# Optimization experiments

Measured on AMD Instinct MI355X. Metric: run time of the kernel, lower is better.

The kernel has to match this reference:

```python
import jax, jax.numpy as jnp
import numpy as np

CHEB_K = 3
EMBED_DIM = 16
N_NODES = 2048
DIM = 64


def setup_inputs() -> dict:
    key = jax.random.key(0)
    k1, k2, k3, k4 = jax.random.split(key, 4)
    B, N, T, D = 16, N_NODES, 12, DIM
    x = jax.random.normal(k1, (B, N, T, D), dtype=jnp.float32)
    node_embeddings = jax.random.normal(k2, (N, EMBED_DIM), dtype=jnp.float32)
    # xavier-uniform-ish init for pools
    wp_bound = float(np.sqrt(6.0 / (EMBED_DIM * CHEB_K * D + D)))
    weights_pool = jax.random.uniform(k3, (EMBED_DIM, CHEB_K, D, D), dtype=jnp.float32,
                                      minval=-wp_bound, maxval=wp_bound)
    bias_pool = jax.random.uniform(k4, (EMBED_DIM, D), dtype=jnp.float32)
    return {"x": x, "node_embeddings": node_embeddings,
            "weights_pool": weights_pool, "bias_pool": bias_pool}


def reference(x, node_embeddings, weights_pool, bias_pool):
    B, N, T, D = x.shape
    cheb_k = weights_pool.shape[1]
    # [B,N,T,D] -> [B*T, N, D]
    xr = jnp.transpose(x, (0, 2, 1, 3)).reshape(B * T, N, D)
    # adaptive adjacency: row-softmax of relu gram matrix  [N,N]
    supports = jax.nn.softmax(jax.nn.relu(node_embeddings @ node_embeddings.T), axis=1)
    # Chebyshev polynomial basis of the adaptive support
    support_set = [jnp.eye(N, dtype=supports.dtype), supports]
    for _ in range(2, cheb_k):
        support_set.append(2.0 * supports @ support_set[-1] - support_set[-2])
    supports_k = jnp.stack(support_set, axis=0)  # [K,N,N]
    # hypernetwork: per-node weights/bias from embeddings
    weights = jnp.einsum('nd,dkio->nkio', node_embeddings, weights_pool)  # [N,K,D,D]
    bias = node_embeddings @ bias_pool  # [N,D]
    # graph conv: gather K-hop aggregates, then per-node grouped GEMM
    x_g = jnp.einsum('knm,bmc->bnkc', supports_k, xr)  # [B*T,N,K,D]
    x_gconv = jnp.einsum('bnki,nkio->bno', x_g, weights) + bias  # [B*T,N,D]
    return jnp.transpose(x_gconv.reshape(B, T, N, D), (0, 2, 1, 3))
```

## Files before the change

### kernel.cpp

```cpp
#include <hip/hip_runtime.h>
#include <hip/hip_bf16.h>

#define N_NODES 2048
#define EMB 16
#define NT 12
#define BT 192
#define C_COLS 12288
#define TD 768
#define BSTRIDE (N_NODES * TD)
#define KDIM 2048

typedef unsigned short u16;
typedef unsigned int u32;
typedef __attribute__((ext_vector_type(8))) __bf16 bf16x8;
typedef __attribute__((ext_vector_type(8))) u16 u16x8;
typedef __attribute__((ext_vector_type(4))) float f32x4;

__device__ __forceinline__ u16 f2bfu(float f) {
    u32 u = __float_as_uint(f);
    return (u16)((u + 0x7FFFu + ((u >> 16) & 1u)) >> 16);
}
__device__ __forceinline__ float bfu2f(u16 h) {
    return __uint_as_float(((u32)h) << 16);
}

__device__ __forceinline__ void gl2lds16(const void* g, void* l) {
    __builtin_amdgcn_global_load_lds(
        (const __attribute__((address_space(1))) u32*)g,
        (__attribute__((address_space(3))) u32*)l, 16, 0, 0);
}

__device__ __forceinline__ int cswz(int col, int row) {
    return (col & ~63) | ((((col >> 3) ^ row) & 7) << 3) | (col & 7);
}

__global__ void supports_kernel(const float* __restrict__ E, u16* __restrict__ Sb)
{
    __shared__ float en[EMB];
    __shared__ float red[256];
    const int n = blockIdx.x;
    const int tid = threadIdx.x;
    if (tid < EMB) en[tid] = E[n * EMB + tid];
    __syncthreads();

    float v[8];
    float mx = 0.0f;
    #pragma unroll
    for (int j = 0; j < 8; ++j) {
        const int m = tid + j * 256;
        const float* em = E + m * EMB;
        float acc = 0.f;
        #pragma unroll
        for (int d = 0; d < EMB; ++d) acc += en[d] * em[d];
        acc = fmaxf(acc, 0.f);
        v[j] = acc;
        mx = fmaxf(mx, acc);
    }
    red[tid] = mx;
    __syncthreads();
    for (int s = 128; s > 0; s >>= 1) {
        if (tid < s) red[tid] = fmaxf(red[tid], red[tid + s]);
        __syncthreads();
    }
    mx = red[0];
    __syncthreads();

    float sum = 0.f;
    #pragma unroll
    for (int j = 0; j < 8; ++j) { v[j] = __expf(v[j] - mx); sum += v[j]; }
    red[tid] = sum;
    __syncthreads();
    for (int s = 128; s > 0; s >>= 1) {
        if (tid < s) red[tid] += red[tid + s];
        __syncthreads();
    }
    const float inv = 1.f / red[0];
    #pragma unroll
    for (int j = 0; j < 8; ++j)
        Sb[(size_t)n * KDIM + tid + j * 256] = f2bfu(v[j] * inv);
}

__global__ void supports2_kernel(const float* __restrict__ E, u16* __restrict__ Sb)
{
    __shared__ float en[EMB];
    __shared__ float red[256];
    const int n = blockIdx.x;
    const int tid = threadIdx.x;
    if (tid < EMB) en[tid] = E[n * EMB + tid];
    __syncthreads();

    float v[8];
    float mx = 0.0f;
    #pragma unroll
    for (int j = 0; j < 8; ++j) {
        const int m = tid + j * 256;
        const float* em = E + m * EMB;
        float acc = 0.f;
        #pragma unroll
        for (int d = 0; d < EMB; ++d) acc += en[d] * em[d];
        acc = fmaxf(acc, 0.f);
        v[j] = acc;
        mx = fmaxf(mx, acc);
    }
    red[tid] = mx;
    __syncthreads();
    for (int s = 128; s > 0; s >>= 1) {
        if (tid < s) red[tid] = fmaxf(red[tid], red[tid + s]);
        __syncthreads();
    }
    mx = red[0];
    __syncthreads();

    float sum = 0.f;
    #pragma unroll
    for (int j = 0; j < 8; ++j) { v[j] = __expf(v[j] - mx); sum += v[j]; }
    red[tid] = sum;
    __syncthreads();
    for (int s = 128; s > 0; s >>= 1) {
        if (tid < s) red[tid] += red[tid + s];
        __syncthreads();
    }
    const float inv = 1.f / red[0];
    #pragma unroll
    for (int j = 0; j < 8; ++j) {
        const int m = tid + j * 256;
        Sb[(size_t)n * KDIM + cswz(m, n)] = f2bfu(v[j] * inv);
    }
}

__global__ void strans_kernel(const u16* __restrict__ Sb, u16* __restrict__ SbT)
{
    __shared__ u16 T[64][65];
    const int tid = threadIdx.x;
    const int n0 = blockIdx.y * 64;
    const int j0 = blockIdx.x * 64;
    const int lc = tid & 63;
    const int rg = tid >> 6;
    #pragma unroll
    for (int j = 0; j < 16; ++j) {
        const int r = j * 4 + rg;
        const u16 vv = Sb[(size_t)(n0 + r) * KDIM + j0 + lc];
        const int jt = ((((lc >> 3) ^ (n0 + r)) & 7) << 3) | (lc & 7);
        T[jt][r] = vv;
    }
    __syncthreads();
    #pragma unroll
    for (int j = 0; j < 16; ++j) {
        const int jj = j * 4 + rg;
        const int cs = ((((lc >> 3) ^ (j0 + jj)) & 7) << 3) | (lc & 7);
        SbT[(size_t)(j0 + jj) * KDIM + n0 + cs] = T[jj][lc];
    }
}

__global__ void xcast_kernel(const float* __restrict__ x, u16* __restrict__ XbT, int c0g)
{
    __shared__ u16 tile[64][65];
    const int tid = threadIdx.x;
    const int cg = c0g + blockIdx.x * 64;
    const int b = cg / TD;
    const int r0 = cg - b * TD;
    const int m0 = blockIdx.y * 64;
    const float* xp = x + (size_t)b * BSTRIDE + (size_t)m0 * TD + r0;

    const int lc = tid & 63;
    const int rg = tid >> 6;
    #pragma unroll
    for (int j = 0; j < 16; ++j) {
        const int mr = j * 4 + rg;
        tile[lc][mr] = f2bfu(xp[(size_t)mr * TD + lc]);
    }
    __syncthreads();
    u16* op = XbT + (size_t)(blockIdx.x * 64) * KDIM + m0;
    #pragma unroll
    for (int j = 0; j < 16; ++j) {
        const int cr = j * 4 + rg;
        op[(size_t)cr * KDIM + lc] = tile[cr][lc];
    }
}

__global__ void xcast2_kernel(const float* __restrict__ x, u16* __restrict__ XbT)
{
    __shared__ u16 tile[64][65];
    const int tid = threadIdx.x;
    const int cg = blockIdx.x * 64;
    const int b = cg / TD;
    const int r0 = cg - b * TD;
    const int m0 = blockIdx.y * 64;
    const float* xp = x + (size_t)b * BSTRIDE + (size_t)m0 * TD + r0;

    const int lc = tid & 63;
    const int rg = tid >> 6;
    #pragma unroll
    for (int j = 0; j < 16; ++j) {
        const int mr = j * 4 + rg;
        tile[lc][mr] = f2bfu(xp[(size_t)mr * TD + lc]);
    }
    __syncthreads();
    u16* op = XbT + (size_t)cg * KDIM + m0;
    #pragma unroll
    for (int j = 0; j < 16; ++j) {
        const int cr = j * 4 + rg;
        const int ls = ((((lc >> 3) ^ cr) & 7) << 3) | (lc & 7);
        op[(size_t)cr * KDIM + ls] = tile[cr][lc];
    }
}

template <int MODE>
__launch_bounds__(512, 2)
__global__ void gemm256(const u16* __restrict__ A, const u16* __restrict__ B,
                        u16* __restrict__ O1, u16* __restrict__ O2)
{
    __shared__ char smem[131072];
    const int tid = threadIdx.x;
    const int lane = tid & 63;
    const int w = tid >> 6;
    const int wm = w >> 2, wn = w & 3;
    const int ln15 = lane & 15, quad = lane >> 4;

    const int m0 = blockIdx.y * 256;
    const int c0 = blockIdx.x * 256;

    const int srow = lane >> 3;
    const int sbyte = (lane & 7) * 16;
    const char* gA = (const char*)A + (size_t)(m0 + w * 32 + srow) * 4096 + sbyte;
    const char* gB = (const char*)B + (size_t)(c0 + w * 32 + srow) * 4096 + sbyte;
    char* lA = smem + w * 4096;
    char* lB = smem + 32768 + w * 4096;

    auto stage = [&](int t, int buf) {
        #pragma unroll
        for (int j = 0; j < 4; ++j) {
            gl2lds16(gA + (size_t)j * 32768 + (size_t)t * 128,
                     lA + buf * 65536 + j * 1024);
            gl2lds16(gB + (size_t)j * 32768 + (size_t)t * 128,
                     lB + buf * 65536 + j * 1024);
        }
    };

    f32x4 acc[8][4] = {};
    const int arow0 = wm * 128 + ln15;
    const int brow0 = wn * 64 + ln15;
    const int xorm = (ln15 & 7) << 4;

    auto phase = [&](const char* Ab, const char* Bb, int kh) {
        const int koff = (kh * 64 + quad * 16) ^ xorm;
        bf16x8 af[8], bg[4];
        #pragma unroll
        for (int mi = 0; mi < 8; ++mi)
            af[mi] = *(const bf16x8*)(Ab + (arow0 + mi * 16) * 128 + koff);
        #pragma unroll
        for (int ni = 0; ni < 4; ++ni)
            bg[ni] = *(const bf16x8*)(Bb + (brow0 + ni * 16) * 128 + koff);
        asm volatile("s_waitcnt lgkmcnt(0)" ::: "memory");
        __builtin_amdgcn_sched_barrier(0);
        __builtin_amdgcn_s_setprio(1);
        #pragma unroll
        for (int mi = 0; mi < 8; ++mi)
            #pragma unroll
            for (int ni = 0; ni < 4; ++ni)
                acc[mi][ni] = __builtin_amdgcn_mfma_f32_16x16x32_bf16(
                    af[mi], bg[ni], acc[mi][ni], 0, 0, 0);
        __builtin_amdgcn_s_setprio(0);
        __builtin_amdgcn_sched_barrier(0);
        __builtin_amdgcn_s_barrier();
    };

    const char* b0A = smem;
    const char* b0B = smem + 32768;
    const char* b1A = smem + 65536;
    const char* b1B = smem + 98304;

    const int NTI = KDIM / 64;
    stage(0, 0);
    stage(1, 1);

    #pragma unroll 1
    for (int it = 0; it < NTI / 2; ++it) {
        const int t0 = 2 * it;
        if (it > 0) stage(t0 + 1, 1);
        asm volatile("s_waitcnt vmcnt(8)" ::: "memory");
        __builtin_amdgcn_sched_barrier(0);
        __builtin_amdgcn_s_barrier();

        phase(b0A, b0B, 0);
        phase(b0A, b0B, 1);

        if (t0 + 2 < NTI) {
            stage(t0 + 2, 0);
            asm volatile("s_waitcnt vmcnt(8)" ::: "memory");
        } else {
            asm volatile("s_waitcnt vmcnt(0)" ::: "memory");
        }
        __builtin_amdgcn_sched_barrier(0);
        __builtin_amdgcn_s_barrier();

        phase(b1A, b1B, 0);
        phase(b1A, b1B, 1);
    }

    const int mbase = m0 + wm * 128 + quad * 4;
    const int cbase = c0 + wn * 64 + ln15;
    if (MODE == 0) {
        #pragma unroll
        for (int mi = 0; mi < 8; ++mi) {
            #pragma unroll
            for (int ni = 0; ni < 4; ++ni) {
                const f32x4 v = acc[mi][ni];
                const int cc = cbase + ni * 16;
                #pragma unroll
                for (int r = 0; r < 4; ++r) {
                    const int mm = mbase + mi * 16 + r;
                    const float t2 = 2.f * v[r] - ((mm == cc) ? 1.f : 0.f);
                    O1[(size_t)mm * KDIM + cswz(cc, mm)] = f2bfu(t2);
                }
            }
        }
    } else {
        u16* Ob = (m0 < 2048) ? O1 : O2;
        const int mb = (m0 < 2048) ? mbase : (mbase - 2048);
        #pragma unroll
        for (int mi = 0; mi < 8; ++mi) {
            #pragma unroll
            for (int ni = 0; ni < 4; ++ni) {
                const f32x4 v = acc[mi][ni];
                const int cc = cbase + ni * 16;
                u16* orow = Ob + (size_t)(mb + mi * 16) * C_COLS + cc;
                orow[0 * C_COLS] = f2bfu(v.x);
                orow[1 * C_COLS] = f2bfu(v.y);
                orow[2 * C_COLS] = f2bfu(v.z);
                orow[3 * C_COLS] = f2bfu(v.w);
            }
        }
    }
}

template <int MODE>
__launch_bounds__(256, 3)
__global__ void mfma_gemm(const u16* __restrict__ A,
                          const u16* __restrict__ B,
                          u16* __restrict__ OutT,
                          u16* __restrict__ OutRow,
                          const u16* __restrict__ Xc,
                          int c0g)
{
    __shared__ char smem[16384];
    char* As = smem;
    char* Bs = smem + 8192;

    const int tid = threadIdx.x;
    const int lane = tid & 63;
    const int w = tid >> 6;
    const int wm = w >> 1, wn = w & 1;
    const int ln15 = lane & 15, quad = lane >> 4;

    const int m0 = blockIdx.y * 128;
    const int cb = blockIdx.x * 128;

    const int q0 = 2 * w, q1 = 2 * w + 1;
    const int srow = lane >> 2;
    const int skol = (lane & 3) * 8;
    const u16* ga0 = A + (size_t)(m0 + q0 * 16 + srow) * KDIM + skol;
    const u16* ga1 = A + (size_t)(m0 + q1 * 16 + srow) * KDIM + skol;
    const u16* gb0 = B + (size_t)(cb + q0 * 16 + srow) * KDIM + skol;
    const u16* gb1 = B + (size_t)(cb + q1 * 16 + srow) * KDIM + skol;
    char* la0 = As + q0 * 1024;
    char* la1 = As + q1 * 1024;
    char* lb0 = Bs + q0 * 1024;
    char* lb1 = Bs + q1 * 1024;

    f32x4 acc[4][4] = {};

    for (int k0 = 0; k0 < KDIM; k0 += 32) {
        __syncthreads();
        gl2lds16(ga0, la0);
        gl2lds16(ga1, la1);
        gl2lds16(gb0, lb0);
        gl2lds16(gb1, lb1);
        ga0 += 32; ga1 += 32; gb0 += 32; gb1 += 32;
        __syncthreads();

        bf16x8 af[4], bg[4];
        #pragma unroll
        for (int i = 0; i < 4; ++i) {
            af[i] = *(const bf16x8*)(As + ((wm * 64 + i * 16 + ln15) * 64 + quad * 16));
            bg[i] = *(const bf16x8*)(Bs + ((wn * 64 + i * 16 + ln15) * 64 + quad * 16));
        }
        #pragma unroll
        for (int mi = 0; mi < 4; ++mi)
            #pragma unroll
            for (int ni = 0; ni < 4; ++ni)
                acc[mi][ni] = __builtin_amdgcn_mfma_f32_16x16x32_bf16(
                    af[mi], bg[ni], acc[mi][ni], 0, 0, 0);
    }

    const int mbase = m0 + wm * 64 + quad * 4;
    const int cbase = cb + wn * 64 + ln15;
    #pragma unroll
    for (int mi = 0; mi < 4; ++mi) {
        #pragma unroll
        for (int ni = 0; ni < 4; ++ni) {
            const f32x4 v = acc[mi][ni];
            const int mm = mbase + mi * 16;
            const int cc = cbase + ni * 16;
            if (MODE == 0) {
                ushort4 u;
                u.x = f2bfu(v.x); u.y = f2bfu(v.y); u.z = f2bfu(v.z); u.w = f2bfu(v.w);
                *(ushort4*)(OutT + (size_t)cc * KDIM + mm) = u;
                u16* orow = OutRow + (size_t)mm * C_COLS + c0g + cc;
                orow[0 * C_COLS] = u.x;
                orow[1 * C_COLS] = u.y;
                orow[2 * C_COLS] = u.z;
                orow[3 * C_COLS] = u.w;
            } else {
                const ushort4 xv = *(const ushort4*)(Xc + (size_t)cc * KDIM + mm);
                u16* orow = OutRow + (size_t)mm * C_COLS + c0g + cc;
                orow[0 * C_COLS] = f2bfu(2.f * v.x - bfu2f(xv.x));
                orow[1 * C_COLS] = f2bfu(2.f * v.y - bfu2f(xv.y));
                orow[2 * C_COLS] = f2bfu(2.f * v.z - bfu2f(xv.z));
                orow[3 * C_COLS] = f2bfu(2.f * v.w - bfu2f(xv.w));
            }
        }
    }
}

__launch_bounds__(256, 2)
__global__ void whyper_kernel(const float* __restrict__ E,
                              const float* __restrict__ Wp,
                              u16* __restrict__ Wrow)
{
    __shared__ float Es[32][16];
    const int tid = threadIdx.x;
    const int kt = blockIdx.x;
    const int n0 = blockIdx.y * 32;
    for (int i = tid; i < 512; i += 256)
        Es[i >> 4][i & 15] = E[(n0 + (i >> 4)) * EMB + (i & 15)];
    __syncthreads();

    const int o = tid & 63;
    const int kq = tid >> 6;
    #pragma unroll 1
    for (int it = 0; it < 6; ++it) {
        const int ki = kt * 24 + it * 4 + kq;
        const float* wp = Wp + (size_t)ki * 64 + o;
        float wv[EMB];
        #pragma unroll
        for (int d = 0; d < EMB; ++d) wv[d] = wp[(size_t)d * 12288];
        #pragma unroll 4
        for (int nn = 0; nn < 32; ++nn) {
            float a = 0.f;
            #pragma unroll
            for (int d = 0; d < EMB; ++d) a = fmaf(Es[nn][d], wv[d], a);
            Wrow[(size_t)(n0 + nn) * 12288 + (size_t)ki * 64 + o] = f2bfu(a);
        }
    }
}

__launch_bounds__(256, 2)
__global__ void wtrans_kernel(u16* __restrict__ Wbuf)
{
    __shared__ u16 Wt[64 * 192];
    const int n = blockIdx.x;
    const int tid = threadIdx.x;
    u16* Wn = Wbuf + (size_t)n * 12288;

    ushort4 va[6][2];
    #pragma unroll
    for (int j = 0; j < 6; ++j) {
        const int c = tid + j * 256;
        va[j][0] = *(const ushort4*)(Wn + c * 8);
        va[j][1] = *(const ushort4*)(Wn + c * 8 + 4);
    }
    #pragma unroll
    for (int j = 0; j < 6; ++j) {
        const int c = tid + j * 256;
        const int ki = c >> 3;
        const int o0 = (c & 7) * 8;
        Wt[(o0 + 0) * 192 + ki] = va[j][0].x;
        Wt[(o0 + 1) * 192 + ki] = va[j][0].y;
        Wt[(o0 + 2) * 192 + ki] = va[j][0].z;
        Wt[(o0 + 3) * 192 + ki] = va[j][0].w;
        Wt[(o0 + 4) * 192 + ki] = va[j][1].x;
        Wt[(o0 + 5) * 192 + ki] = va[j][1].y;
        Wt[(o0 + 6) * 192 + ki] = va[j][1].z;
        Wt[(o0 + 7) * 192 + ki] = va[j][1].w;
    }
    __syncthreads();

    #pragma unroll
    for (int j = 0; j < 6; ++j) {
        const int c = tid + j * 256;
        const int o = c / 24;
        const int kc = c - o * 24;
        const int ki0 = kc * 8;
        const int m = (o & 7) << 4;
        const ushort4 lo = *(const ushort4*)(Wt + o * 192 + ki0);
        const ushort4 hi = *(const ushort4*)(Wt + o * 192 + ki0 + 4);
        char* gp = (char*)Wbuf + (size_t)n * 24576 + o * 384 + ((ki0 * 2) ^ m);
        *(ushort4*)gp = lo;
        *(ushort4*)(gp + 8) = hi;
    }
}

__launch_bounds__(256, 4)
__global__ void gconv_mfma2_kernel(const float* __restrict__ x,
                                   const float* __restrict__ E,
                                   const float* __restrict__ Bp,
                                   const u16* __restrict__ Wall,
                                   const u16* __restrict__ Y1,
                                   const u16* __restrict__ Y2,
                                   float* __restrict__ Out)
{
    __shared__ char WsB[24576];
    __shared__ float en[EMB];
    __shared__ float bias[64];

    const int n = blockIdx.x;
    const int tid = threadIdx.x;
    const int lane = tid & 63;
    const int w = tid >> 6;

    if (tid < EMB) en[tid] = E[n * EMB + tid];

    const char* Wn = (const char*)Wall + (size_t)n * 24576;
    for (int iss = w; iss < 24; iss += 4)
        gl2lds16(Wn + iss * 1024 + lane * 16, WsB + iss * 1024);

    __syncthreads();

    if (tid < 64) {
        float a = 0.f;
        #pragma unroll
        for (int d = 0; d < EMB; ++d) a = fmaf(en[d], Bp[d * 64 + tid], a);
        bias[tid] = a;
    }
    __syncthreads();

    const int ln15 = lane & 15, quad = lane >> 4;
    const int q16 = quad * 16;
    const int m0w = w * 48;

    int rowb[4], msk[4];
    #pragma unroll
    for (int ni = 0; ni < 4; ++ni) {
        const int o = ni * 16 + ln15;
        rowb[ni] = o * 384;
        msk[ni] = (o & 7) << 4;
    }

    const float* xb[3];
    size_t yo[3];
    #pragma unroll
    for (int mi = 0; mi < 3; ++mi) {
        const int bt = m0w + mi * 16 + ln15;
        const int b = bt / NT, t = bt - b * NT;
        xb[mi] = x + (size_t)b * BSTRIDE + (size_t)n * TD + (size_t)t * 64 + quad * 8;
        yo[mi] = (size_t)n * C_COLS + (size_t)bt * 64 + quad * 8;
    }

    f32x4 acc[3][4] = {};

    #pragma unroll
    for (int ks = 0; ks < 2; ++ks) {
        bf16x8 af[3];
        #pragma unroll
        for (int mi = 0; mi < 3; ++mi) {
            const float* p = xb[mi] + ks * 32;
            const f32x4 lo = *(const f32x4*)p;
            const f32x4 hi = *(const f32x4*)(p + 4);
            u16x8 u;
            u[0] = f2bfu(lo.x); u[1] = f2bfu(lo.y); u[2] = f2bfu(lo.z); u[3] = f2bfu(lo.w);
            u[4] = f2bfu(hi.x); u[5] = f2bfu(hi.y); u[6] = f2bfu(hi.z); u[7] = f2bfu(hi.w);
            af[mi] = *(const bf16x8*)&u;
        }
        bf16x8 bg[4];
        #pragma unroll
        for (int ni = 0; ni < 4; ++ni)
            bg[ni] = *(const bf16x8*)(WsB + rowb[ni] + ((ks * 64 + q16) ^ msk[ni]));
        #pragma unroll
        for (int mi = 0; mi < 3; ++mi)
            #pragma unroll
            for (int ni = 0; ni < 4; ++ni)
                acc[mi][ni] = __builtin_amdgcn_mfma_f32_16x16x32_bf16(
                    af[mi], bg[ni], acc[mi][ni], 0, 0, 0);
    }

    const u16* ybase[2] = { Y1, Y2 };
    #pragma unroll
    for (int s = 0; s < 2; ++s) {
        const u16* Yb = ybase[s];
        #pragma unroll
        for (int ks = 0; ks < 2; ++ks) {
            bf16x8 af[3];
            #pragma unroll
            for (int mi = 0; mi < 3; ++mi)
                af[mi] = *(const bf16x8*)(Yb + yo[mi] + ks * 32);
            bf16x8 bg[4];
            #pragma unroll
            for (int ni = 0; ni < 4; ++ni)
                bg[ni] = *(const bf16x8*)(WsB + rowb[ni] + 128 + s * 128
                                          + ((ks * 64 + q16) ^ msk[ni]));
            #pragma unroll
            for (int mi = 0; mi < 3; ++mi)
                #pragma unroll
                for (int ni = 0; ni < 4; ++ni)
                    acc[mi][ni] = __builtin_amdgcn_mfma_f32_16x16x32_bf16(
                        af[mi], bg[ni], acc[mi][ni], 0, 0, 0);
        }
    }

    float bv[4];
    #pragma unroll
    for (int ni = 0; ni < 4; ++ni) bv[ni] = bias[ni * 16 + ln15];

    #pragma unroll
    for (int mi = 0; mi < 3; ++mi) {
        const int rowb2 = m0w + mi * 16 + quad * 4;
        #pragma unroll
        for (int r = 0; r < 4; ++r) {
            const int bt = rowb2 + r;
            const int b = bt / NT, t = bt - b * NT;
            float* op = Out + (((size_t)(b * N_NODES + n)) * NT + t) * 64 + ln15;
            #pragma unroll
            for (int ni = 0; ni < 4; ++ni)
                op[ni * 16] = acc[mi][ni][r] + bv[ni];
        }
    }
}

__launch_bounds__(256, 4)
__global__ void gconv_mfma_kernel(const float* __restrict__ x,
                                  const float* __restrict__ E,
                                  const float* __restrict__ Wp,
                                  const float* __restrict__ Bp,
                                  const u16* __restrict__ Y1,
                                  const u16* __restrict__ Y2,
                                  float* __restrict__ Out)
{
    __shared__ u16 Ws[64][200];
    __shared__ float en[EMB];
    __shared__ float bias[64];

    const int n = blockIdx.x;
    const int tid = threadIdx.x;
    if (tid < EMB) en[tid] = E[n * EMB + tid];
    __syncthreads();

    {
        const int o = tid & 63;
        const int kio = tid >> 6;
        #pragma unroll 4
        for (int j = 0; j < 48; ++j) {
            const int ki = j * 4 + kio;
            const float* wp = Wp + ki * 64 + o;
            float a = 0.f;
            #pragma unroll
            for (int d = 0; d < EMB; ++d) a = fmaf(en[d], wp[d * 12288], a);
            Ws[o][ki] = f2bfu(a);
        }
        if (tid < 64) {
            float a = 0.f;
            #pragma unroll
            for (int d = 0; d < EMB; ++d) a = fmaf(en[d], Bp[d * 64 + tid], a);
            bias[tid] = a;
        }
    }
    __syncthreads();

    const int lane = tid & 63;
    const int w = tid >> 6;
    const int ln15 = lane & 15, quad = lane >> 4;
    const int m0w = w * 48;

    const float* xb[3];
    size_t yo[3];
    #pragma unroll
    for (int mi = 0; mi < 3; ++mi) {
        const int bt = m0w + mi * 16 + ln15;
        const int b = bt / NT, t = bt - b * NT;
        xb[mi] = x + (size_t)b * BSTRIDE + (size_t)n * TD + (size_t)t * 64 + quad * 8;
        yo[mi] = (size_t)n * C_COLS + (size_t)bt * 64 + quad * 8;
    }

    f32x4 acc[3][4] = {};

    #pragma unroll
    for (int ks = 0; ks < 2; ++ks) {
        bf16x8 af[3];
        #pragma unroll
        for (int mi = 0; mi < 3; ++mi) {
            const float* p = xb[mi] + ks * 32;
            const f32x4 lo = *(const f32x4*)p;
            const f32x4 hi = *(const f32x4*)(p + 4);
            u16x8 u;
            u[0] = f2bfu(lo.x); u[1] = f2bfu(lo.y); u[2] = f2bfu(lo.z); u[3] = f2bfu(lo.w);
            u[4] = f2bfu(hi.x); u[5] = f2bfu(hi.y); u[6] = f2bfu(hi.z); u[7] = f2bfu(hi.w);
            af[mi] = *(const bf16x8*)&u;
        }
        bf16x8 bg[4];
        #pragma unroll
        for (int ni = 0; ni < 4; ++ni)
            bg[ni] = *(const bf16x8*)&Ws[ni * 16 + ln15][ks * 32 + quad * 8];
        #pragma unroll
        for (int mi = 0; mi < 3; ++mi)
            #pragma unroll
            for (int ni = 0; ni < 4; ++ni)
                acc[mi][ni] = __builtin_amdgcn_mfma_f32_16x16x32_bf16(
                    af[mi], bg[ni], acc[mi][ni], 0, 0, 0);
    }

    const u16* ybase[2] = { Y1, Y2 };
    #pragma unroll
    for (int s = 0; s < 2; ++s) {
        const u16* Yb = ybase[s];
        #pragma unroll
        for (int ks = 0; ks < 2; ++ks) {
            bf16x8 af[3];
            #pragma unroll
            for (int mi = 0; mi < 3; ++mi)
                af[mi] = *(const bf16x8*)(Yb + yo[mi] + ks * 32);
            bf16x8 bg[4];
            #pragma unroll
            for (int ni = 0; ni < 4; ++ni)
                bg[ni] = *(const bf16x8*)&Ws[ni * 16 + ln15][64 + s * 64 + ks * 32 + quad * 8];
            #pragma unroll
            for (int mi = 0; mi < 3; ++mi)
                #pragma unroll
                for (int ni = 0; ni < 4; ++ni)
                    acc[mi][ni] = __builtin_amdgcn_mfma_f32_16x16x32_bf16(
                        af[mi], bg[ni], acc[mi][ni], 0, 0, 0);
        }
    }

    float bv[4];
    #pragma unroll
    for (int ni = 0; ni < 4; ++ni) bv[ni] = bias[ni * 16 + ln15];

    #pragma unroll
    for (int mi = 0; mi < 3; ++mi) {
        const int rowb = m0w + mi * 16 + quad * 4;
        #pragma unroll
        for (int r = 0; r < 4; ++r) {
            const int bt = rowb + r;
            const int b = bt / NT, t = bt - b * NT;
            float* op = Out + (((size_t)(b * N_NODES + n)) * NT + t) * 64 + ln15;
            #pragma unroll
            for (int ni = 0; ni < 4; ++ni)
                op[ni * 16] = acc[mi][ni][r] + bv[ni];
        }
    }
}

extern "C" void kernel_launch(void* const* d_in, const int* in_sizes, int n_in,
                              void* d_out, int out_size, void* d_ws, size_t ws_size,
                              hipStream_t stream)
{
    const float* x  = (const float*)d_in[0];
    const float* E  = (const float*)d_in[1];
    const float* Wp = (const float*)d_in[2];
    const float* Bp = (const float*)d_in[3];
    float* Out = (float*)d_out;

    const size_t MiB = 1024 * 1024;

    if (ws_size >= 216 * MiB) {
        u16* Sb    = (u16*)d_ws;
        u16* T2b   = (u16*)((char*)d_ws + 8 * MiB);
        u16* SbT   = (u16*)((char*)d_ws + 16 * MiB);
        u16* Y1row = (u16*)((char*)d_ws + 24 * MiB);
        u16* Y2row = (u16*)((char*)d_ws + 72 * MiB);
        u16* XbT   = (u16*)((char*)d_ws + 120 * MiB);
        u16* Wbuf  = (u16*)((char*)d_ws + 168 * MiB);

        supports2_kernel<<<N_NODES, 256, 0, stream>>>(E, Sb);
        strans_kernel<<<dim3(32, 32), 256, 0, stream>>>(Sb, SbT);
        gemm256<0><<<dim3(8, 8), 512, 0, stream>>>(Sb, SbT, T2b, nullptr);
        xcast2_kernel<<<dim3(192, 32), 256, 0, stream>>>(x, XbT);
        gemm256<1><<<dim3(48, 16), 512, 0, stream>>>(Sb, XbT, Y1row, Y2row);

        whyper_kernel<<<dim3(8, 64), 256, 0, stream>>>(E, Wp, Wbuf);
        wtrans_kernel<<<N_NODES, 256, 0, stream>>>(Wbuf);
        gconv_mfma2_kernel<<<N_NODES, 256, 0, stream>>>(x, E, Bp, Wbuf, Y1row, Y2row, Out);
        return;
    }

    u16* Sb    = (u16*)d_ws;
    u16* Y1row = (u16*)((char*)d_ws + 8 * MiB);
    u16* Y2row = (u16*)((char*)d_ws + 56 * MiB);
    char* chunkbase = (char*)d_ws + 104 * MiB;

    size_t wall_off = 0;
    bool newpath = false;
    if (ws_size >= 160 * MiB) {
        wall_off = ((ws_size - 48 * MiB) / 256) * 256;
        if (wall_off >= 112 * MiB) newpath = true;
    }
    const size_t budget = newpath ? wall_off : ws_size;

    const int cands[5] = {1, 2, 3, 6, 12};
    int nc = 12;
    for (int i = 0; i < 5; ++i) {
        const size_t chunk_bytes = (size_t)(C_COLS / cands[i]) * KDIM * 2;
        if (104 * MiB + 2 * chunk_bytes <= budget) { nc = cands[i]; break; }
    }
    const int CW = C_COLS / nc;
    u16* XbTc = (u16*)chunkbase;
    u16* Y1Tc = (u16*)(chunkbase + (size_t)CW * KDIM * 2);
    u16* Wbuf = (u16*)((char*)d_ws + wall_off);

    supports_kernel<<<N_NODES, 256, 0, stream>>>(E, Sb);

    if (newpath) {
        whyper_kernel<<<dim3(8, 64), 256, 0, stream>>>(E, Wp, Wbuf);
        wtrans_kernel<<<N_NODES, 256, 0, stream>>>(Wbuf);
    }

    for (int c = 0; c < nc; ++c) {
        const int c0g = c * CW;
        xcast_kernel<<<dim3(CW / 64, 32), 256, 0, stream>>>(x, XbTc, c0g);
        mfma_gemm<0><<<dim3(CW / 128, 16), 256, 0, stream>>>(Sb, XbTc, Y1Tc, Y1row, nullptr, c0g);
        mfma_gemm<1><<<dim3(CW / 128, 16), 256, 0, stream>>>(Sb, Y1Tc, nullptr, Y2row, XbTc, c0g);
    }

    if (newpath)
        gconv_mfma2_kernel<<<N_NODES, 256, 0, stream>>>(x, E, Bp, Wbuf, Y1row, Y2row, Out);
    else
        gconv_mfma_kernel<<<N_NODES, 256, 0, stream>>>(x, E, Wp, Bp, Y1row, Y2row, Out);
}
```

Before: 544.2 us.

## Fuse weight transpose into gconv and use 128-tile GEMM for T2

Removes the separate wtrans kernel and performs the per-node weight transpose and swizzle directly into LDS inside gconv_mfma2, reading row-major hypernetwork weights with plain loads instead of async global-to-LDS copies. The S·S^T Chebyshev GEMM is switched from a 256x256-tile kernel on an 8x8 grid to a new 128x128-tile, double-buffered kernel on a 16x16 grid, giving more blocks to fill the CUs. The trade-offs are scalar 16-bit LDS stores in gconv, which may cause bank conflicts, and the smaller GEMM tile reduces data reuse per block.

```diff
diff --git a/kernel.cpp b/kernel.cpp
--- a/kernel.cpp
+++ b/kernel.cpp
@@ -329,6 +329,111 @@
                 orow[1 * C_COLS] = f2bfu(v.y);
                 orow[2 * C_COLS] = f2bfu(v.z);
                 orow[3 * C_COLS] = f2bfu(v.w);
+            }
+        }
+    }
+}
+
+__launch_bounds__(256, 2)
+__global__ void gemm128s(const u16* __restrict__ A, const u16* __restrict__ B,
+                         u16* __restrict__ O1)
+{
+    __shared__ char smem[65536];
+    const int tid = threadIdx.x;
+    const int lane = tid & 63;
+    const int w = tid >> 6;
+    const int wm = w >> 1, wn = w & 1;
+    const int ln15 = lane & 15, quad = lane >> 4;
+
+    const int m0 = blockIdx.y * 128;
+    const int c0 = blockIdx.x * 128;
+
+    const int srow = lane >> 3;
+    const int sbyte = (lane & 7) * 16;
+    const char* gA = (const char*)A + (size_t)(m0 + w * 32 + srow) * 4096 + sbyte;
+    const char* gB = (const char*)B + (size_t)(c0 + w * 32 + srow) * 4096 + sbyte;
+    char* lA = smem + w * 4096;
+    char* lB = smem + 16384 + w * 4096;
+
+    auto stage = [&](int t, int buf) {
+        #pragma unroll
+        for (int j = 0; j < 4; ++j) {
+            gl2lds16(gA + (size_t)j * 32768 + (size_t)t * 128,
+                     lA + buf * 32768 + j * 1024);
+            gl2lds16(gB + (size_t)j * 32768 + (size_t)t * 128,
+                     lB + buf * 32768 + j * 1024);
+        }
+    };
+
+    f32x4 acc[4][4] = {};
+    const int arow0 = wm * 64 + ln15;
+    const int brow0 = wn * 64 + ln15;
+    const int xorm = (ln15 & 7) << 4;
+
+    auto phase = [&](const char* Ab, const char* Bb, int kh) {
+        const int koff = (kh * 64 + quad * 16) ^ xorm;
+        bf16x8 af[4], bg[4];
+        #pragma unroll
+        for (int mi = 0; mi < 4; ++mi)
+            af[mi] = *(const bf16x8*)(Ab + (arow0 + mi * 16) * 128 + koff);
+        #pragma unroll
+        for (int ni = 0; ni < 4; ++ni)
+            bg[ni] = *(const bf16x8*)(Bb + (brow0 + ni * 16) * 128 + koff);
+        asm volatile("s_waitcnt lgkmcnt(0)" ::: "memory");
+        __builtin_amdgcn_sched_barrier(0);
+        __builtin_amdgcn_s_setprio(1);
+        #pragma unroll
+        for (int mi = 0; mi < 4; ++mi)
+            #pragma unroll
+            for (int ni = 0; ni < 4; ++ni)
+                acc[mi][ni] = __builtin_amdgcn_mfma_f32_16x16x32_bf16(
+                    af[mi], bg[ni], acc[mi][ni], 0, 0, 0);
+        __builtin_amdgcn_s_setprio(0);
+        __builtin_amdgcn_sched_barrier(0);
+        __builtin_amdgcn_s_barrier();
+    };
+
+    const int NTI = KDIM / 64;
+    stage(0, 0);
+    stage(1, 1);
+
+    #pragma unroll 1
+    for (int it = 0; it < NTI / 2; ++it) {
+        const int t0 = 2 * it;
+        if (it > 0) stage(t0 + 1, 1);
+        asm volatile("s_waitcnt vmcnt(8)" ::: "memory");
+        __builtin_amdgcn_sched_barrier(0);
+        __builtin_amdgcn_s_barrier();
+
+        phase(smem, smem + 16384, 0);
+        phase(smem, smem + 16384, 1);
+
+        if (t0 + 2 < NTI) {
+            stage(t0 + 2, 0);
+            asm volatile("s_waitcnt vmcnt(8)" ::: "memory");
+        } else {
+            asm volatile("s_waitcnt vmcnt(0)" ::: "memory");
+        }
+        __builtin_amdgcn_sched_barrier(0);
+        __builtin_amdgcn_s_barrier();
+
+        phase(smem + 32768, smem + 49152, 0);
+        phase(smem + 32768, smem + 49152, 1);
+    }
+
+    const int mbase = m0 + wm * 64 + quad * 4;
+    const int cbase = c0 + wn * 64 + ln15;
+    #pragma unroll
+    for (int mi = 0; mi < 4; ++mi) {
+        #pragma unroll
+        for (int ni = 0; ni < 4; ++ni) {
+            const f32x4 v = acc[mi][ni];
+            const int cc = cbase + ni * 16;
+            #pragma unroll
+            for (int r = 0; r < 4; ++r) {
+                const int mm = mbase + mi * 16 + r;
+                const float t2 = 2.f * v[r] - ((mm == cc) ? 1.f : 0.f);
+                O1[(size_t)mm * KDIM + cswz(cc, mm)] = f2bfu(t2);
             }
         }
     }
@@ -455,57 +560,11 @@
     }
 }
 
-__launch_bounds__(256, 2)
-__global__ void wtrans_kernel(u16* __restrict__ Wbuf)
-{
-    __shared__ u16 Wt[64 * 192];
-    const int n = blockIdx.x;
-    const int tid = threadIdx.x;
-    u16* Wn = Wbuf + (size_t)n * 12288;
-
-    ushort4 va[6][2];
-    #pragma unroll
-    for (int j = 0; j < 6; ++j) {
-        const int c = tid + j * 256;
-        va[j][0] = *(const ushort4*)(Wn + c * 8);
-        va[j][1] = *(const ushort4*)(Wn + c * 8 + 4);
-    }
-    #pragma unroll
-    for (int j = 0; j < 6; ++j) {
-        const int c = tid + j * 256;
-        const int ki = c >> 3;
-        const int o0 = (c & 7) * 8;
-        Wt[(o0 + 0) * 192 + ki] = va[j][0].x;
-        Wt[(o0 + 1) * 192 + ki] = va[j][0].y;
-        Wt[(o0 + 2) * 192 + ki] = va[j][0].z;
-        Wt[(o0 + 3) * 192 + ki] = va[j][0].w;
-        Wt[(o0 + 4) * 192 + ki] = va[j][1].x;
-        Wt[(o0 + 5) * 192 + ki] = va[j][1].y;
-        Wt[(o0 + 6) * 192 + ki] = va[j][1].z;
-        Wt[(o0 + 7) * 192 + ki] = va[j][1].w;
-    }
-    __syncthreads();
-
-    #pragma unroll
-    for (int j = 0; j < 6; ++j) {
-        const int c = tid + j * 256;
-        const int o = c / 24;
-        const int kc = c - o * 24;
-        const int ki0 = kc * 8;
-        const int m = (o & 7) << 4;
-        const ushort4 lo = *(const ushort4*)(Wt + o * 192 + ki0);
-        const ushort4 hi = *(const ushort4*)(Wt + o * 192 + ki0 + 4);
-        char* gp = (char*)Wbuf + (size_t)n * 24576 + o * 384 + ((ki0 * 2) ^ m);
-        *(ushort4*)gp = lo;
-        *(ushort4*)(gp + 8) = hi;
-    }
-}
-
 __launch_bounds__(256, 4)
 __global__ void gconv_mfma2_kernel(const float* __restrict__ x,
                                    const float* __restrict__ E,
                                    const float* __restrict__ Bp,
-                                   const u16* __restrict__ Wall,
+                                   const u16* __restrict__ Wrow,
                                    const u16* __restrict__ Y1,
                                    const u16* __restrict__ Y2,
                                    float* __restrict__ Out)
@@ -521,10 +580,30 @@
 
     if (tid < EMB) en[tid] = E[n * EMB + tid];
 
-    const char* Wn = (const char*)Wall + (size_t)n * 24576;
-    for (int iss = w; iss < 24; iss += 4)
-        gl2lds16(Wn + iss * 1024 + lane * 16, WsB + iss * 1024);
-
+    {
+        const u16* Wn = Wrow + (size_t)n * 12288;
+        ushort4 va[6][2];
+        #pragma unroll
+        for (int j = 0; j < 6; ++j) {
+            const int c = tid + j * 256;
+            va[j][0] = *(const ushort4*)(Wn + c * 8);
+            va[j][1] = *(const ushort4*)(Wn + c * 8 + 4);
+        }
+        #pragma unroll
+        for (int j = 0; j < 6; ++j) {
+            const int c = tid + j * 256;
+            const int ki = c >> 3;
+            const int o0 = (c & 7) * 8;
+            const int kb = ((ki >> 3) << 4) | ((ki & 7) * 2);
+            const u16 vals[8] = { va[j][0].x, va[j][0].y, va[j][0].z, va[j][0].w,
+                                  va[j][1].x, va[j][1].y, va[j][1].z, va[j][1].w };
+            #pragma unroll
+            for (int e = 0; e < 8; ++e) {
+                const int o = o0 + e;
+                *(u16*)(WsB + o * 384 + (kb ^ ((o & 7) << 4))) = vals[e];
+            }
+        }
+    }
     __syncthreads();
 
     if (tid < 64) {
@@ -773,12 +852,11 @@
 
         supports2_kernel<<<N_NODES, 256, 0, stream>>>(E, Sb);
         strans_kernel<<<dim3(32, 32), 256, 0, stream>>>(Sb, SbT);
-        gemm256<0><<<dim3(8, 8), 512, 0, stream>>>(Sb, SbT, T2b, nullptr);
+        gemm128s<<<dim3(16, 16), 256, 0, stream>>>(Sb, SbT, T2b);
         xcast2_kernel<<<dim3(192, 32), 256, 0, stream>>>(x, XbT);
         gemm256<1><<<dim3(48, 16), 512, 0, stream>>>(Sb, XbT, Y1row, Y2row);
 
         whyper_kernel<<<dim3(8, 64), 256, 0, stream>>>(E, Wp, Wbuf);
-        wtrans_kernel<<<N_NODES, 256, 0, stream>>>(Wbuf);
         gconv_mfma2_kernel<<<N_NODES, 256, 0, stream>>>(x, E, Bp, Wbuf, Y1row, Y2row, Out);
         return;
     }
@@ -811,7 +889,6 @@
 
     if (newpath) {
         whyper_kernel<<<dim3(8, 64), 256, 0, stream>>>(E, Wp, Wbuf);
-        wtrans_kernel<<<N_NODES, 256, 0, stream>>>(Wbuf);
     }
 
     for (int c = 0; c < nc; ++c) {
```

Result: faster. 492.0 us (-9.6%).
